# Optimization experiments

Measured on AMD Instinct MI355X. Metric: run time of the kernel, lower is better.

Reference implementation:

```python
import jax, jax.numpy as jnp
import numpy as np

N, A, C, FM, M = 64, 5, 20, 52, 32


def smooth_l1(a, b):
    d = a - b
    ad = jnp.abs(d)
    return jnp.where(ad < 1.0, 0.5 * d * d, ad - 0.5)


def pairwise_iou_max(boxes_p, boxes_t):
    # boxes_p: [P,4] xyxy, boxes_t: [M,4] xyxy -> max IoU over targets, [P]
    lt = jnp.maximum(boxes_p[:, None, :2], boxes_t[None, :, :2])
    rb = jnp.minimum(boxes_p[:, None, 2:], boxes_t[None, :, 2:])
    wh = jnp.clip(rb - lt, 0.0)
    inter = wh[..., 0] * wh[..., 1]
    area_p = (boxes_p[:, 2] - boxes_p[:, 0]) * (boxes_p[:, 3] - boxes_p[:, 1])
    area_t = (boxes_t[:, 2] - boxes_t[:, 0]) * (boxes_t[:, 3] - boxes_t[:, 1])
    iou = inter / (area_p[:, None] + area_t[None, :] - inter)
    return jnp.max(iou, axis=1)


def setup_inputs() -> dict:
    key = jax.random.key(0)
    k1, k2, k3, k4, k5, k6 = jax.random.split(key, 6)
    preds = jax.random.normal(k1, (N, A * (5 + C), FM, FM), jnp.float32)
    loc_targets = jax.random.uniform(k2, (N, A, 4, FM, FM), jnp.float32) * 2.0
    # sparse positive class targets (most cells background -> zeros)
    cls_raw = jax.random.uniform(k3, (N, A, C, FM, FM), jnp.float32)
    keep = (jax.random.uniform(k4, (N, A, C, FM, FM)) < 0.05).astype(jnp.float32)
    cls_targets = cls_raw * keep
    # ground-truth boxes in feature-map coordinates, xyxy with positive wh
    cxy = jax.random.uniform(k5, (N, M, 2), jnp.float32) * FM
    wh = jax.random.uniform(k6, (N, M, 2), jnp.float32) * 8.0 + 1.0
    box_targets = jnp.concatenate([cxy - 0.5 * wh, cxy + 0.5 * wh], axis=-1)
    anchors = jnp.asarray(
        [[1.3221, 1.73145], [3.19275, 4.00944], [5.05587, 8.09892],
         [9.47112, 4.84053], [11.2364, 10.0071]], jnp.float32)
    return {"preds": preds, "loc_targets": loc_targets,
            "cls_targets": cls_targets, "box_targets": box_targets,
            "anchors": anchors}


def reference(preds, loc_targets, cls_targets, box_targets, anchors):
    n, _, fm, _ = preds.shape
    p = preds.reshape(n, A, 5 + C, fm, fm)
    xy = jax.nn.sigmoid(p[:, :, :2])          # [N,A,2,fm,fm]
    wh = jnp.exp(p[:, :, 2:4])                # [N,A,2,fm,fm]
    loc_preds = jnp.concatenate([xy, wh], axis=2)

    pos = jnp.max(cls_targets, axis=2) > 0    # [N,A,fm,fm]
    num_pos = jnp.sum(pos).astype(jnp.float32)

    loc_mask = pos[:, :, None, :, :].astype(loc_preds.dtype)
    loc_loss = jnp.sum(smooth_l1(loc_preds, loc_targets) * loc_mask)

    # decode boxes: xy + grid offset, wh * anchor, then xyxy
    gx = jnp.arange(fm, dtype=preds.dtype)
    grid = jnp.stack(jnp.meshgrid(gx, gx, indexing="xy"), axis=0)  # [2,fm,fm]
    box_xy = xy + grid[None, None]                                   # [N,A,2,fm,fm]
    box_wh = anchors[None, :, :, None, None] * wh                    # [N,A,2,fm,fm]
    boxes = jnp.concatenate([box_xy - 0.5 * box_wh, box_xy + 0.5 * box_wh], axis=2)
    box_preds = boxes.transpose(0, 1, 3, 4, 2).reshape(n, -1, 4)     # [N,A*fm*fm,4]

    iou_targets = jax.vmap(pairwise_iou_max)(box_preds, box_targets)
    iou_targets = iou_targets.reshape(n, A, fm, fm)
    iou_preds = jax.nn.sigmoid(p[:, :, 4])
    iou_mask = jnp.where(pos, 1.0, 0.1).astype(iou_preds.dtype)
    iou_loss = jnp.sum(smooth_l1(iou_preds * iou_mask, iou_targets * iou_mask))

    cls_logits = p[:, :, 5:].transpose(0, 1, 3, 4, 2)   # [N,A,fm,fm,C]
    cls_preds = jax.nn.softmax(cls_logits, axis=-1).transpose(0, 1, 4, 2, 3)
    cls_mask = (cls_targets > 0).astype(cls_preds.dtype)
    cls_loss = jnp.sum(smooth_l1(cls_preds, cls_targets) * cls_mask)

    return (loc_loss + iou_loss + cls_loss) / num_pos
```

## Files before the change

kernel.cpp:

```cpp
#include <hip/hip_runtime.h>

#define N_IMG 64
#define NA 5
#define NC 20
#define FM 52
#define NM 32
#define FMFM (FM * FM)
#define CELLS_PER_IMG (NA * FMFM)
#define BLOCK 256
#define BLOCKS_PER_IMG ((CELLS_PER_IMG + BLOCK - 1) / BLOCK)

__device__ __forceinline__ float smooth_l1(float a, float b) {
    float d = a - b;
    float ad = fabsf(d);
    return ad < 1.0f ? 0.5f * d * d : ad - 0.5f;
}

__global__ __launch_bounds__(BLOCK) void yolo_loss_main(
    const float* __restrict__ preds,
    const float* __restrict__ loc_t,
    const float* __restrict__ cls_t,
    const float* __restrict__ box_t,
    const float* __restrict__ anchors,
    double* __restrict__ acc)
{
    __shared__ float sbox[NM * 4];
    __shared__ float sarea[NM];
    __shared__ double wsum[BLOCK / 64];
    __shared__ double wpos[BLOCK / 64];

    const int n = blockIdx.y;
    const int tid = threadIdx.x;

    if (tid < NM * 4) sbox[tid] = box_t[n * NM * 4 + tid];
    __syncthreads();
    if (tid < NM) {
        float x1 = sbox[tid * 4 + 0], y1 = sbox[tid * 4 + 1];
        float x2 = sbox[tid * 4 + 2], y2 = sbox[tid * 4 + 3];
        sarea[tid] = (x2 - x1) * (y2 - y1);
    }
    __syncthreads();

    const int cell = blockIdx.x * BLOCK + tid;
    float loss = 0.0f;
    float posf = 0.0f;

    if (cell < CELLS_PER_IMG) {
        const int a = cell / FMFM;
        const int rem = cell - a * FMFM;
        const int y = rem / FM;
        const int x = rem - y * FM;

        const float* pbase = preds + (size_t)(n * NA + a) * 25 * FMFM + rem;
        float p[25];
        #pragma unroll
        for (int ch = 0; ch < 25; ++ch) p[ch] = pbase[ch * FMFM];

        const float* cbase = cls_t + (size_t)(n * NA + a) * NC * FMFM + rem;
        float ct[NC];
        float cmax = 0.0f;
        #pragma unroll
        for (int c = 0; c < NC; ++c) { ct[c] = cbase[c * FMFM]; cmax = fmaxf(cmax, ct[c]); }
        const bool pos = cmax > 0.0f;
        posf = pos ? 1.0f : 0.0f;

        float sx = 1.0f / (1.0f + expf(-p[0]));
        float sy = 1.0f / (1.0f + expf(-p[1]));
        float ew = expf(p[2]);
        float eh = expf(p[3]);

        if (pos) {
            const float* lbase = loc_t + (size_t)(n * NA + a) * 4 * FMFM + rem;
            loss += smooth_l1(sx, lbase[0 * FMFM]);
            loss += smooth_l1(sy, lbase[1 * FMFM]);
            loss += smooth_l1(ew, lbase[2 * FMFM]);
            loss += smooth_l1(eh, lbase[3 * FMFM]);
        }

        float aw = anchors[a * 2 + 0], ah = anchors[a * 2 + 1];
        float bx = sx + (float)x;
        float by = sy + (float)y;
        float bw = aw * ew, bh = ah * eh;
        float px1 = bx - 0.5f * bw, py1 = by - 0.5f * bh;
        float px2 = bx + 0.5f * bw, py2 = by + 0.5f * bh;
        float area_p = (px2 - px1) * (py2 - py1);

        float best = -1e30f;
        #pragma unroll 8
        for (int t = 0; t < NM; ++t) {
            float lx = fmaxf(px1, sbox[t * 4 + 0]);
            float ly = fmaxf(py1, sbox[t * 4 + 1]);
            float rx = fminf(px2, sbox[t * 4 + 2]);
            float ry = fminf(py2, sbox[t * 4 + 3]);
            float w = fmaxf(rx - lx, 0.0f);
            float h = fmaxf(ry - ly, 0.0f);
            float inter = w * h;
            float iou = inter / (area_p + sarea[t] - inter);
            best = fmaxf(best, iou);
        }

        float iou_pred = 1.0f / (1.0f + expf(-p[4]));
        float mask = pos ? 1.0f : 0.1f;
        loss += smooth_l1(iou_pred * mask, best * mask);

        float m = p[5];
        #pragma unroll
        for (int c = 1; c < NC; ++c) m = fmaxf(m, p[5 + c]);
        float e[NC];
        float s = 0.0f;
        #pragma unroll
        for (int c = 0; c < NC; ++c) { e[c] = expf(p[5 + c] - m); s += e[c]; }
        float inv = 1.0f / s;
        #pragma unroll
        for (int c = 0; c < NC; ++c) {
            if (ct[c] > 0.0f) loss += smooth_l1(e[c] * inv, ct[c]);
        }
    }

    double dl = (double)loss;
    double dp = (double)posf;
    #pragma unroll
    for (int off = 32; off > 0; off >>= 1) {
        dl += __shfl_down(dl, off);
        dp += __shfl_down(dp, off);
    }
    const int wave = tid >> 6, lane = tid & 63;
    if (lane == 0) { wsum[wave] = dl; wpos[wave] = dp; }
    __syncthreads();
    if (tid == 0) {
        double tl = 0.0, tp = 0.0;
        #pragma unroll
        for (int w = 0; w < BLOCK / 64; ++w) { tl += wsum[w]; tp += wpos[w]; }
        atomicAdd(&acc[0], tl);
        atomicAdd(&acc[1], tp);
    }
}

__global__ void yolo_loss_finalize(const double* __restrict__ acc,
                                   float* __restrict__ out) {
    out[0] = (float)(acc[0] / acc[1]);
}

extern "C" void kernel_launch(void* const* d_in, const int* in_sizes, int n_in,
                              void* d_out, int out_size, void* d_ws, size_t ws_size,
                              hipStream_t stream) {
    const float* preds   = (const float*)d_in[0];
    const float* loc_t   = (const float*)d_in[1];
    const float* cls_t   = (const float*)d_in[2];
    const float* box_t   = (const float*)d_in[3];
    const float* anchors = (const float*)d_in[4];
    double* acc = (double*)d_ws;

    hipMemsetAsync(d_ws, 0, 2 * sizeof(double), stream);

    dim3 grid(BLOCKS_PER_IMG, N_IMG);
    yolo_loss_main<<<grid, BLOCK, 0, stream>>>(preds, loc_t, cls_t, box_t,
                                               anchors, acc);
    yolo_loss_finalize<<<1, 1, 0, stream>>>(acc, (float*)d_out);
}
```

Before: 247.2 us.

## Process four cells per thread with float4 loads and division-free IoU max

Each thread now handles four adjacent cells and loads every channel with float4 vector loads, so the kernel issues fewer, wider memory transactions. The IoU max is tracked as an inter/denominator pair compared by cross-multiplication, which removes the per-target division. Exponentials and reciprocals use fast intrinsics, class targets are reread instead of held in registers, and launch bounds request occupancy 3. In exchange there are more registers per thread, fewer threads overall, and slightly lower precision from the fast math.

```diff
diff --git a/kernel.cpp b/kernel.cpp
--- a/kernel.cpp
+++ b/kernel.cpp
@@ -6,17 +6,26 @@
 #define FM 52
 #define NM 32
 #define FMFM (FM * FM)
+#define Q (FMFM / 4)
 #define CELLS_PER_IMG (NA * FMFM)
+#define T_PER_IMG (CELLS_PER_IMG / 4)
 #define BLOCK 256
-#define BLOCKS_PER_IMG ((CELLS_PER_IMG + BLOCK - 1) / BLOCK)
-
-__device__ __forceinline__ float smooth_l1(float a, float b) {
+#define BX ((T_PER_IMG + BLOCK - 1) / BLOCK)
+
+__device__ __forceinline__ float fast_rcp(float x) { return __builtin_amdgcn_rcpf(x); }
+
+__device__ __forceinline__ float sl1(float a, float b) {
     float d = a - b;
     float ad = fabsf(d);
     return ad < 1.0f ? 0.5f * d * d : ad - 0.5f;
 }
 
-__global__ __launch_bounds__(BLOCK) void yolo_loss_main(
+__device__ __forceinline__ void ld4(const float4* p, float o[4]) {
+    float4 v = *p;
+    o[0] = v.x; o[1] = v.y; o[2] = v.z; o[3] = v.w;
+}
+
+__global__ __launch_bounds__(BLOCK, 3) void yolo_loss_main(
     const float* __restrict__ preds,
     const float* __restrict__ loc_t,
     const float* __restrict__ cls_t,
@@ -24,7 +33,7 @@
     const float* __restrict__ anchors,
     double* __restrict__ acc)
 {
-    __shared__ float sbox[NM * 4];
+    __shared__ __align__(16) float sbox[NM * 4];
     __shared__ float sarea[NM];
     __shared__ double wsum[BLOCK / 64];
     __shared__ double wpos[BLOCK / 64];
@@ -41,84 +50,123 @@
     }
     __syncthreads();
 
-    const int cell = blockIdx.x * BLOCK + tid;
+    const int t = blockIdx.x * BLOCK + tid;
     float loss = 0.0f;
-    float posf = 0.0f;
-
-    if (cell < CELLS_PER_IMG) {
-        const int a = cell / FMFM;
-        const int rem = cell - a * FMFM;
-        const int y = rem / FM;
-        const int x = rem - y * FM;
-
-        const float* pbase = preds + (size_t)(n * NA + a) * 25 * FMFM + rem;
-        float p[25];
-        #pragma unroll
-        for (int ch = 0; ch < 25; ++ch) p[ch] = pbase[ch * FMFM];
-
-        const float* cbase = cls_t + (size_t)(n * NA + a) * NC * FMFM + rem;
-        float ct[NC];
-        float cmax = 0.0f;
-        #pragma unroll
-        for (int c = 0; c < NC; ++c) { ct[c] = cbase[c * FMFM]; cmax = fmaxf(cmax, ct[c]); }
-        const bool pos = cmax > 0.0f;
-        posf = pos ? 1.0f : 0.0f;
-
-        float sx = 1.0f / (1.0f + expf(-p[0]));
-        float sy = 1.0f / (1.0f + expf(-p[1]));
-        float ew = expf(p[2]);
-        float eh = expf(p[3]);
-
-        if (pos) {
-            const float* lbase = loc_t + (size_t)(n * NA + a) * 4 * FMFM + rem;
-            loss += smooth_l1(sx, lbase[0 * FMFM]);
-            loss += smooth_l1(sy, lbase[1 * FMFM]);
-            loss += smooth_l1(ew, lbase[2 * FMFM]);
-            loss += smooth_l1(eh, lbase[3 * FMFM]);
-        }
-
-        float aw = anchors[a * 2 + 0], ah = anchors[a * 2 + 1];
-        float bx = sx + (float)x;
-        float by = sy + (float)y;
-        float bw = aw * ew, bh = ah * eh;
-        float px1 = bx - 0.5f * bw, py1 = by - 0.5f * bh;
-        float px2 = bx + 0.5f * bw, py2 = by + 0.5f * bh;
-        float area_p = (px2 - px1) * (py2 - py1);
-
-        float best = -1e30f;
-        #pragma unroll 8
-        for (int t = 0; t < NM; ++t) {
-            float lx = fmaxf(px1, sbox[t * 4 + 0]);
-            float ly = fmaxf(py1, sbox[t * 4 + 1]);
-            float rx = fminf(px2, sbox[t * 4 + 2]);
-            float ry = fminf(py2, sbox[t * 4 + 3]);
-            float w = fmaxf(rx - lx, 0.0f);
-            float h = fmaxf(ry - ly, 0.0f);
-            float inter = w * h;
-            float iou = inter / (area_p + sarea[t] - inter);
-            best = fmaxf(best, iou);
-        }
-
-        float iou_pred = 1.0f / (1.0f + expf(-p[4]));
-        float mask = pos ? 1.0f : 0.1f;
-        loss += smooth_l1(iou_pred * mask, best * mask);
-
-        float m = p[5];
-        #pragma unroll
-        for (int c = 1; c < NC; ++c) m = fmaxf(m, p[5 + c]);
-        float e[NC];
-        float s = 0.0f;
-        #pragma unroll
-        for (int c = 0; c < NC; ++c) { e[c] = expf(p[5 + c] - m); s += e[c]; }
-        float inv = 1.0f / s;
+    float posn = 0.0f;
+
+    if (t < T_PER_IMG) {
+        const int g = t * 4;
+        const int a = g / FMFM;
+        const int rem = g - a * FMFM;
+        const int yy = rem / FM;
+        const int xx = rem - yy * FM;
+
+        const float4* pb = (const float4*)(preds + (size_t)(n * NA + a) * 25 * FMFM + rem);
+        const float4* cb = (const float4*)(cls_t + (size_t)(n * NA + a) * NC * FMFM + rem);
+        const float4* lb = (const float4*)(loc_t + (size_t)(n * NA + a) * 4  * FMFM + rem);
+
+        float l[NC][4];
+        #pragma unroll
+        for (int c = 0; c < NC; ++c) ld4(pb + (5 + c) * Q, l[c]);
+
+        float m[4] = { l[0][0], l[0][1], l[0][2], l[0][3] };
+        #pragma unroll
+        for (int c = 1; c < NC; ++c) {
+            #pragma unroll
+            for (int j = 0; j < 4; ++j) m[j] = fmaxf(m[j], l[c][j]);
+        }
+
+        float cmax[4] = {0.f, 0.f, 0.f, 0.f};
+        float s[4] = {0.f, 0.f, 0.f, 0.f};
         #pragma unroll
         for (int c = 0; c < NC; ++c) {
-            if (ct[c] > 0.0f) loss += smooth_l1(e[c] * inv, ct[c]);
+            float tv[4]; ld4(cb + c * Q, tv);
+            #pragma unroll
+            for (int j = 0; j < 4; ++j) {
+                cmax[j] = fmaxf(cmax[j], tv[j]);
+                float e = __expf(l[c][j] - m[j]);
+                s[j] += e;
+                l[c][j] = e;
+            }
+        }
+
+        float posf[4], iouw[4];
+        #pragma unroll
+        for (int j = 0; j < 4; ++j) {
+            bool p = cmax[j] > 0.0f;
+            posf[j] = p ? 1.0f : 0.0f;
+            iouw[j] = p ? 1.0f : 0.1f;
+            posn += posf[j];
+        }
+
+        float P0[4], P1[4], P2[4], P3[4], P4[4], T0[4], T1[4], T2[4], T3[4];
+        ld4(pb + 0 * Q, P0); ld4(pb + 1 * Q, P1); ld4(pb + 2 * Q, P2);
+        ld4(pb + 3 * Q, P3); ld4(pb + 4 * Q, P4);
+        ld4(lb + 0 * Q, T0); ld4(lb + 1 * Q, T1);
+        ld4(lb + 2 * Q, T2); ld4(lb + 3 * Q, T3);
+
+        const float aw = anchors[a * 2 + 0];
+        const float ah = anchors[a * 2 + 1];
+
+        float px1[4], py1[4], px2[4], py2[4], ap[4], ib[4], db[4];
+        #pragma unroll
+        for (int j = 0; j < 4; ++j) {
+            float sx = fast_rcp(1.0f + __expf(-P0[j]));
+            float sy = fast_rcp(1.0f + __expf(-P1[j]));
+            float ew = __expf(P2[j]);
+            float eh = __expf(P3[j]);
+            loss += posf[j] * (sl1(sx, T0[j]) + sl1(sy, T1[j]) +
+                               sl1(ew, T2[j]) + sl1(eh, T3[j]));
+            float bx = sx + (float)(xx + j);
+            float by = sy + (float)yy;
+            float bw = aw * ew, bh = ah * eh;
+            px1[j] = bx - 0.5f * bw; py1[j] = by - 0.5f * bh;
+            px2[j] = bx + 0.5f * bw; py2[j] = by + 0.5f * bh;
+            ap[j] = (px2[j] - px1[j]) * (py2[j] - py1[j]);
+            ib[j] = 0.0f; db[j] = 1.0f;
+        }
+
+        #pragma unroll 4
+        for (int tb = 0; tb < NM; ++tb) {
+            float b0 = sbox[tb * 4 + 0], b1 = sbox[tb * 4 + 1];
+            float b2 = sbox[tb * 4 + 2], b3 = sbox[tb * 4 + 3];
+            float sa = sarea[tb];
+            #pragma unroll
+            for (int j = 0; j < 4; ++j) {
+                float lx = fmaxf(px1[j], b0), ly = fmaxf(py1[j], b1);
+                float rx = fminf(px2[j], b2), ry = fminf(py2[j], b3);
+                float w = fmaxf(rx - lx, 0.0f), h = fmaxf(ry - ly, 0.0f);
+                float inter = w * h;
+                float den = ap[j] + sa - inter;
+                bool gt = inter * db[j] > ib[j] * den;
+                ib[j] = gt ? inter : ib[j];
+                db[j] = gt ? den   : db[j];
+            }
+        }
+
+        #pragma unroll
+        for (int j = 0; j < 4; ++j) {
+            float best = ib[j] * fast_rcp(db[j]);
+            float ip = fast_rcp(1.0f + __expf(-P4[j]));
+            loss += sl1(ip * iouw[j], best * iouw[j]);
+        }
+
+        float inv[4];
+        #pragma unroll
+        for (int j = 0; j < 4; ++j) inv[j] = fast_rcp(s[j]);
+        #pragma unroll
+        for (int c = 0; c < NC; ++c) {
+            float tv[4]; ld4(cb + c * Q, tv);
+            #pragma unroll
+            for (int j = 0; j < 4; ++j) {
+                float v = sl1(l[c][j] * inv[j], tv[j]);
+                loss += tv[j] > 0.0f ? v : 0.0f;
+            }
         }
     }
 
     double dl = (double)loss;
-    double dp = (double)posf;
+    double dp = (double)posn;
     #pragma unroll
     for (int off = 32; off > 0; off >>= 1) {
         dl += __shfl_down(dl, off);
@@ -153,7 +201,7 @@
 
     hipMemsetAsync(d_ws, 0, 2 * sizeof(double), stream);
 
-    dim3 grid(BLOCKS_PER_IMG, N_IMG);
+    dim3 grid(BX, N_IMG);
     yolo_loss_main<<<grid, BLOCK, 0, stream>>>(preds, loc_t, cls_t, box_t,
                                                anchors, acc);
     yolo_loss_finalize<<<1, 1, 0, stream>>>(acc, (float*)d_out);
```

Measured after the change: 263.1 us. 1.06x slower.

## Process four cells per thread with float4 loads and division-free IoU max

Applied to the files above, without the earlier changes.

Each thread now handles four adjacent cells, loading preds, class targets and loc targets as float4 vectors to cut load instruction count and improve coalescing. The IoU max avoids per-target division by tracking the best numerator/denominator pair through cross-multiplication, with one reciprocal at the end. Exact expf and divisions are replaced with fast __expf and hardware rcp, and loc loss is computed unconditionally and multiplied by a mask. This raises register pressure from holding 20 float4 logits, and the fast math intrinsics give slightly lower precision.

```diff
diff --git a/kernel.cpp b/kernel.cpp
--- a/kernel.cpp
+++ b/kernel.cpp
@@ -6,25 +6,60 @@
 #define FM 52
 #define NM 32
 #define FMFM (FM * FM)
-#define CELLS_PER_IMG (NA * FMFM)
+#define Q (FMFM / 4)
+#define CELLS (NA * FMFM)
+#define TPI (CELLS / 4)
 #define BLOCK 256
-#define BLOCKS_PER_IMG ((CELLS_PER_IMG + BLOCK - 1) / BLOCK)
+#define BX ((TPI + BLOCK - 1) / BLOCK)
 
-__device__ __forceinline__ float smooth_l1(float a, float b) {
+__device__ __forceinline__ float frcp(float x) { return __builtin_amdgcn_rcpf(x); }
+__device__ __forceinline__ float sl1(float a, float b) {
     float d = a - b;
     float ad = fabsf(d);
     return ad < 1.0f ? 0.5f * d * d : ad - 0.5f;
 }
 
-__global__ __launch_bounds__(BLOCK) void yolo_loss_main(
+#define HEADJ(C, JX) {                                                        \
+    float sx = frcp(1.0f + __expf(-P0.C));                                    \
+    float sy = frcp(1.0f + __expf(-P1.C));                                    \
+    float ew = __expf(P2.C);                                                  \
+    float eh = __expf(P3.C);                                                  \
+    loss += pos.C * (sl1(sx, T0.C) + sl1(sy, T1.C) +                          \
+                     sl1(ew, T2.C) + sl1(eh, T3.C));                          \
+    float bx = sx + (float)(xx + JX);                                         \
+    float by = sy + (float)yy;                                                \
+    float bw = aw * ew, bh = ah * eh;                                         \
+    px1.C = bx - 0.5f * bw; py1.C = by - 0.5f * bh;                           \
+    px2.C = bx + 0.5f * bw; py2.C = by + 0.5f * bh;                           \
+    ap.C = (px2.C - px1.C) * (py2.C - py1.C);                                 \
+}
+
+#define IOUJ(C) {                                                             \
+    float lx = fmaxf(px1.C, B.x), ly = fmaxf(py1.C, B.y);                     \
+    float rx = fminf(px2.C, B.z), ry = fminf(py2.C, B.w);                     \
+    float w_ = fmaxf(rx - lx, 0.0f), h_ = fmaxf(ry - ly, 0.0f);               \
+    float it = w_ * h_;                                                       \
+    float dn = ap.C + sa - it;                                                \
+    bool gt = it * db.C > ib.C * dn;                                          \
+    ib.C = gt ? it : ib.C;                                                    \
+    db.C = gt ? dn : db.C;                                                    \
+}
+
+#define IOULOSSJ(C) {                                                         \
+    float best  = ib.C * frcp(db.C);                                          \
+    float ipred = frcp(1.0f + __expf(-P4.C));                                 \
+    loss += sl1(ipred * wgt.C, best * wgt.C);                                 \
+}
+
+__global__ __launch_bounds__(BLOCK, 4) void yolo_loss_main(
     const float* __restrict__ preds,
     const float* __restrict__ loc_t,
     const float* __restrict__ cls_t,
-    const float* __restrict__ box_t,
+    const float4* __restrict__ box_t,
     const float* __restrict__ anchors,
     double* __restrict__ acc)
 {
-    __shared__ float sbox[NM * 4];
+    __shared__ float4 sbox[NM];
     __shared__ float sarea[NM];
     __shared__ double wsum[BLOCK / 64];
     __shared__ double wpos[BLOCK / 64];
@@ -32,93 +67,92 @@
     const int n = blockIdx.y;
     const int tid = threadIdx.x;
 
-    if (tid < NM * 4) sbox[tid] = box_t[n * NM * 4 + tid];
-    __syncthreads();
     if (tid < NM) {
-        float x1 = sbox[tid * 4 + 0], y1 = sbox[tid * 4 + 1];
-        float x2 = sbox[tid * 4 + 2], y2 = sbox[tid * 4 + 3];
-        sarea[tid] = (x2 - x1) * (y2 - y1);
+        float4 b = box_t[n * NM + tid];
+        sbox[tid] = b;
+        sarea[tid] = (b.z - b.x) * (b.w - b.y);
     }
     __syncthreads();
 
-    const int cell = blockIdx.x * BLOCK + tid;
+    const int t = blockIdx.x * BLOCK + tid;
     float loss = 0.0f;
-    float posf = 0.0f;
+    float posn = 0.0f;
 
-    if (cell < CELLS_PER_IMG) {
-        const int a = cell / FMFM;
-        const int rem = cell - a * FMFM;
-        const int y = rem / FM;
-        const int x = rem - y * FM;
+    if (t < TPI) {
+        const int g   = t * 4;
+        const int a   = g / FMFM;
+        const int rem = g - a * FMFM;
+        const int yy  = rem / FM;
+        const int xx  = rem - yy * FM;
+        const int q   = rem >> 2;
 
-        const float* pbase = preds + (size_t)(n * NA + a) * 25 * FMFM + rem;
-        float p[25];
+        const float4* pb = (const float4*)(preds + (size_t)(n * NA + a) * 25 * FMFM) + q;
+        const float4* cb = (const float4*)(cls_t + (size_t)(n * NA + a) * NC * FMFM) + q;
+        const float4* lb = (const float4*)(loc_t + (size_t)(n * NA + a) * 4  * FMFM) + q;
+
+        float4 l[NC];
         #pragma unroll
-        for (int ch = 0; ch < 25; ++ch) p[ch] = pbase[ch * FMFM];
+        for (int c = 0; c < NC; ++c) l[c] = pb[(5 + c) * Q];
 
-        const float* cbase = cls_t + (size_t)(n * NA + a) * NC * FMFM + rem;
-        float ct[NC];
-        float cmax = 0.0f;
+        float4 m = l[0];
         #pragma unroll
-        for (int c = 0; c < NC; ++c) { ct[c] = cbase[c * FMFM]; cmax = fmaxf(cmax, ct[c]); }
-        const bool pos = cmax > 0.0f;
-        posf = pos ? 1.0f : 0.0f;
-
-        float sx = 1.0f / (1.0f + expf(-p[0]));
-        float sy = 1.0f / (1.0f + expf(-p[1]));
-        float ew = expf(p[2]);
-        float eh = expf(p[3]);
-
-        if (pos) {
-            const float* lbase = loc_t + (size_t)(n * NA + a) * 4 * FMFM + rem;
-            loss += smooth_l1(sx, lbase[0 * FMFM]);
-            loss += smooth_l1(sy, lbase[1 * FMFM]);
-            loss += smooth_l1(ew, lbase[2 * FMFM]);
-            loss += smooth_l1(eh, lbase[3 * FMFM]);
+        for (int c = 1; c < NC; ++c) {
+            m.x = fmaxf(m.x, l[c].x); m.y = fmaxf(m.y, l[c].y);
+            m.z = fmaxf(m.z, l[c].z); m.w = fmaxf(m.w, l[c].w);
         }
 
-        float aw = anchors[a * 2 + 0], ah = anchors[a * 2 + 1];
-        float bx = sx + (float)x;
-        float by = sy + (float)y;
-        float bw = aw * ew, bh = ah * eh;
-        float px1 = bx - 0.5f * bw, py1 = by - 0.5f * bh;
-        float px2 = bx + 0.5f * bw, py2 = by + 0.5f * bh;
-        float area_p = (px2 - px1) * (py2 - py1);
-
-        float best = -1e30f;
-        #pragma unroll 8
-        for (int t = 0; t < NM; ++t) {
-            float lx = fmaxf(px1, sbox[t * 4 + 0]);
-            float ly = fmaxf(py1, sbox[t * 4 + 1]);
-            float rx = fminf(px2, sbox[t * 4 + 2]);
-            float ry = fminf(py2, sbox[t * 4 + 3]);
-            float w = fmaxf(rx - lx, 0.0f);
-            float h = fmaxf(ry - ly, 0.0f);
-            float inter = w * h;
-            float iou = inter / (area_p + sarea[t] - inter);
-            best = fmaxf(best, iou);
-        }
-
-        float iou_pred = 1.0f / (1.0f + expf(-p[4]));
-        float mask = pos ? 1.0f : 0.1f;
-        loss += smooth_l1(iou_pred * mask, best * mask);
-
-        float m = p[5];
-        #pragma unroll
-        for (int c = 1; c < NC; ++c) m = fmaxf(m, p[5 + c]);
-        float e[NC];
-        float s = 0.0f;
-        #pragma unroll
-        for (int c = 0; c < NC; ++c) { e[c] = expf(p[5 + c] - m); s += e[c]; }
-        float inv = 1.0f / s;
+        float4 s = make_float4(0.f, 0.f, 0.f, 0.f);
         #pragma unroll
         for (int c = 0; c < NC; ++c) {
-            if (ct[c] > 0.0f) loss += smooth_l1(e[c] * inv, ct[c]);
+            s.x += __expf(l[c].x - m.x); s.y += __expf(l[c].y - m.y);
+            s.z += __expf(l[c].z - m.z); s.w += __expf(l[c].w - m.w);
         }
+        float4 inv;
+        inv.x = frcp(s.x); inv.y = frcp(s.y); inv.z = frcp(s.z); inv.w = frcp(s.w);
+
+        float4 cmax = make_float4(0.f, 0.f, 0.f, 0.f);
+        #pragma unroll
+        for (int c = 0; c < NC; ++c) {
+            float4 tv = cb[c * Q];
+            cmax.x = fmaxf(cmax.x, tv.x); cmax.y = fmaxf(cmax.y, tv.y);
+            cmax.z = fmaxf(cmax.z, tv.z); cmax.w = fmaxf(cmax.w, tv.w);
+            loss += tv.x > 0.0f ? sl1(__expf(l[c].x - m.x) * inv.x, tv.x) : 0.0f;
+            loss += tv.y > 0.0f ? sl1(__expf(l[c].y - m.y) * inv.y, tv.y) : 0.0f;
+            loss += tv.z > 0.0f ? sl1(__expf(l[c].z - m.z) * inv.z, tv.z) : 0.0f;
+            loss += tv.w > 0.0f ? sl1(__expf(l[c].w - m.w) * inv.w, tv.w) : 0.0f;
+        }
+        __builtin_amdgcn_sched_barrier(0);
+
+        float4 pos, wgt;
+        pos.x = cmax.x > 0.0f ? 1.0f : 0.0f;  wgt.x = cmax.x > 0.0f ? 1.0f : 0.1f;
+        pos.y = cmax.y > 0.0f ? 1.0f : 0.0f;  wgt.y = cmax.y > 0.0f ? 1.0f : 0.1f;
+        pos.z = cmax.z > 0.0f ? 1.0f : 0.0f;  wgt.z = cmax.z > 0.0f ? 1.0f : 0.1f;
+        pos.w = cmax.w > 0.0f ? 1.0f : 0.0f;  wgt.w = cmax.w > 0.0f ? 1.0f : 0.1f;
+        posn = pos.x + pos.y + pos.z + pos.w;
+
+        float4 P0 = pb[0 * Q], P1 = pb[1 * Q], P2 = pb[2 * Q];
+        float4 P3 = pb[3 * Q], P4 = pb[4 * Q];
+        float4 T0 = lb[0 * Q], T1 = lb[1 * Q], T2 = lb[2 * Q], T3 = lb[3 * Q];
+
+        const float aw = anchors[a * 2 + 0];
+        const float ah = anchors[a * 2 + 1];
+
+        float4 px1, py1, px2, py2, ap, ib, db;
+        HEADJ(x, 0) HEADJ(y, 1) HEADJ(z, 2) HEADJ(w, 3)
+        ib = make_float4(0.f, 0.f, 0.f, 0.f);
+        db = make_float4(1.f, 1.f, 1.f, 1.f);
+
+        #pragma unroll 4
+        for (int tb = 0; tb < NM; ++tb) {
+            float4 B = sbox[tb];
+            float sa = sarea[tb];
+            IOUJ(x) IOUJ(y) IOUJ(z) IOUJ(w)
+        }
+        IOULOSSJ(x) IOULOSSJ(y) IOULOSSJ(z) IOULOSSJ(w)
     }
 
     double dl = (double)loss;
-    double dp = (double)posf;
+    double dp = (double)posn;
     #pragma unroll
     for (int off = 32; off > 0; off >>= 1) {
         dl += __shfl_down(dl, off);
@@ -144,16 +178,16 @@
 extern "C" void kernel_launch(void* const* d_in, const int* in_sizes, int n_in,
                               void* d_out, int out_size, void* d_ws, size_t ws_size,
                               hipStream_t stream) {
-    const float* preds   = (const float*)d_in[0];
-    const float* loc_t   = (const float*)d_in[1];
-    const float* cls_t   = (const float*)d_in[2];
-    const float* box_t   = (const float*)d_in[3];
-    const float* anchors = (const float*)d_in[4];
+    const float*  preds   = (const float*)d_in[0];
+    const float*  loc_t   = (const float*)d_in[1];
+    const float*  cls_t   = (const float*)d_in[2];
+    const float4* box_t   = (const float4*)d_in[3];
+    const float*  anchors = (const float*)d_in[4];
     double* acc = (double*)d_ws;
 
     hipMemsetAsync(d_ws, 0, 2 * sizeof(double), stream);
 
-    dim3 grid(BLOCKS_PER_IMG, N_IMG);
+    dim3 grid(BX, N_IMG);
     yolo_loss_main<<<grid, BLOCK, 0, stream>>>(preds, loc_t, cls_t, box_t,
                                                anchors, acc);
     yolo_loss_finalize<<<1, 1, 0, stream>>>(acc, (float*)d_out);
```

Result: slower. 260.3 us (+5.3%).
